# Kernel optimization log

Hardware: AMD Instinct MI355X
Metric: run time of the kernel (lower is better)

The kernel has to match this reference:

```python
import jax, jax.numpy as jnp
import numpy as np

B, N, M, C, H = 8, 1024, 128, 1024, 16
D = C // H
MLP = int(C * 4.0)
EPS = 1e-6


def setup_inputs() -> dict:
    key = jax.random.key(0)
    ks = jax.random.split(key, 24)
    def w(k, shape):
        return jax.random.normal(k, shape, jnp.float32) * 0.02
    mask = jax.random.randint(ks[3], (B, M), 0, 2, dtype=jnp.int32)
    mask = mask.at[:, 0].set(1)  # ensure at least one attendable token per row
    return {
        "x": jax.random.normal(ks[0], (B, N, C), jnp.float32),
        "c_dino": jax.random.normal(ks[1], (B, C), jnp.float32),
        "c_text": jax.random.normal(ks[2], (B, M, C), jnp.float32),
        "text_mask": mask,
        "W_ada": w(ks[4], (C, 6 * C)), "b_ada": jnp.zeros((6 * C,), jnp.float32),
        "W_qkv": w(ks[5], (C, 3 * C)), "b_qkv": jnp.zeros((3 * C,), jnp.float32),
        "W_proj_sa": w(ks[6], (C, C)), "b_proj_sa": jnp.zeros((C,), jnp.float32),
        "W_q": w(ks[7], (C, C)), "b_q": jnp.zeros((C,), jnp.float32),
        "W_kv": w(ks[8], (C, 2 * C)), "b_kv": jnp.zeros((2 * C,), jnp.float32),
        "W_proj_ca": w(ks[9], (C, C)), "b_proj_ca": jnp.zeros((C,), jnp.float32),
        "W_fc1": w(ks[10], (C, MLP)), "b_fc1": jnp.zeros((MLP,), jnp.float32),
        "W_fc2": w(ks[11], (MLP, C)), "b_fc2": jnp.zeros((C,), jnp.float32),
    }


def _ln(x):
    # LayerNorm without affine params, eps=1e-6
    mu = jnp.mean(x, axis=-1, keepdims=True)
    xc = x - mu
    var = jnp.mean(xc * xc, axis=-1, keepdims=True)
    return xc * jax.lax.rsqrt(var + EPS)


def _modulate(x, shift, scale):
    return x * (1.0 + scale[:, None, :]) + shift[:, None, :]


def _heads(t):
    b, n, _ = t.shape
    return t.reshape(b, n, H, D)


def reference(x, c_dino, c_text, text_mask,
              W_ada, b_ada, W_qkv, b_qkv, W_proj_sa, b_proj_sa,
              W_q, b_q, W_kv, b_kv, W_proj_ca, b_proj_ca,
              W_fc1, b_fc1, W_fc2, b_fc2):
    scale = D ** (-0.5)
    ada = jax.nn.silu(c_dino) @ W_ada + b_ada  # (B, 6C)
    sh_msa, sc_msa, sh_ca, sc_ca, sh_mlp, sc_mlp = jnp.split(ada, 6, axis=1)

    # --- self-attention ---
    h = _modulate(_ln(x), sh_msa, sc_msa)
    qkv = h @ W_qkv + b_qkv
    q, k, v = (_heads(t) for t in jnp.split(qkv, 3, axis=-1))  # (B,N,H,D)
    attn = jax.nn.softmax(jnp.einsum('bnhd,bmhd->bhnm', q, k) * scale, axis=-1)
    sa = jnp.einsum('bhnm,bmhd->bnhd', attn, v).reshape(B, N, C) @ W_proj_sa + b_proj_sa
    x = x + sa

    # --- cross-attention ---
    h = _modulate(_ln(x), sh_ca, sc_ca)
    q = _heads(h @ W_q + b_q)                 # (B,N,H,D)
    kv = c_text @ W_kv + b_kv
    k, v = (_heads(t) for t in jnp.split(kv, 2, axis=-1))  # (B,M,H,D)
    scores = jnp.einsum('bnhd,bmhd->bhnm', q, k) * scale
    scores = jnp.where(text_mask[:, None, None, :] == 0, -jnp.inf, scores)
    attn = jax.nn.softmax(scores, axis=-1)
    ca = jnp.einsum('bhnm,bmhd->bnhd', attn, v).reshape(B, N, C) @ W_proj_ca + b_proj_ca
    x = x + ca

    # --- MLP ---
    h = _modulate(_ln(x), sh_mlp, sc_mlp)
    mlp = jax.nn.gelu(h @ W_fc1 + b_fc1, approximate=True) @ W_fc2 + b_fc2
    return x + mlp
```

## Files before the change

kernel.cpp:

```cpp
#include <hip/hip_runtime.h>
#include <hip/hip_bf16.h>

#define B_   8
#define N_   1024
#define M_   128
#define C_   1024
#define H_   16
#define D_   64
#define MLP_ 4096

typedef __bf16 bf16;
typedef __bf16 bf16x8 __attribute__((ext_vector_type(8)));
typedef __bf16 bf16x4 __attribute__((ext_vector_type(4)));
typedef float  f32x4  __attribute__((ext_vector_type(4)));

__device__ __forceinline__ f32x4 mfma16(bf16x8 a, bf16x8 b, f32x4 c) {
    return __builtin_amdgcn_mfma_f32_16x16x32_bf16(a, b, c, 0, 0, 0);
}

__device__ __forceinline__ void gload16(const bf16* g, bf16* l) {
    __builtin_amdgcn_global_load_lds(
        (const __attribute__((address_space(1))) void*)g,
        (__attribute__((address_space(3))) void*)l, 16, 0, 0);
}

__global__ __launch_bounds__(256) void transpose_k(const float* __restrict__ W,
                                                   bf16* __restrict__ Wt,
                                                   int K, int Nc) {
    __shared__ float tile[32][33];
    const int x  = threadIdx.x & 31;
    const int y0 = threadIdx.x >> 5;
    const size_t n0 = (size_t)blockIdx.x * 32;
    const size_t k0 = (size_t)blockIdx.y * 32;
#pragma unroll
    for (int i = 0; i < 4; i++)
        tile[y0 + i * 8][x] = W[(k0 + y0 + i * 8) * Nc + n0 + x];
    __syncthreads();
#pragma unroll
    for (int i = 0; i < 4; i++)
        Wt[(n0 + y0 + i * 8) * K + k0 + x] = (bf16)tile[x][y0 + i * 8];
}

__global__ __launch_bounds__(256) void vtrans_k(const bf16* __restrict__ in, int instride,
                                                int coff, int Mk, bf16* __restrict__ outT) {
    __shared__ bf16 t[32][33];
    const int tx = threadIdx.x & 31;
    const int ty0 = threadIdx.x >> 5;
    const int m0  = blockIdx.x * 32;
    const int hd0 = blockIdx.y * 32;
    const int b   = blockIdx.z;
#pragma unroll
    for (int i = 0; i < 4; i++)
        t[ty0 + i * 8][tx] = in[((size_t)(b * Mk + m0 + ty0 + i * 8)) * instride + coff + hd0 + tx];
    __syncthreads();
#pragma unroll
    for (int i = 0; i < 4; i++)
        outT[((size_t)(b * 1024 + hd0 + ty0 + i * 8)) * Mk + m0 + tx] = t[tx][ty0 + i * 8];
}

__global__ __launch_bounds__(256) void cvt_bf16_k(const float* __restrict__ in,
                                                  bf16* __restrict__ out, int n4) {
    int i = blockIdx.x * 256 + threadIdx.x;
    if (i < n4) {
        float4 v = ((const float4*)in)[i];
        bf16x4 o;
        o[0] = (bf16)v.x; o[1] = (bf16)v.y; o[2] = (bf16)v.z; o[3] = (bf16)v.w;
        ((bf16x4*)out)[i] = o;
    }
}

__global__ __launch_bounds__(256) void ada_init_k(const float* __restrict__ bias,
                                                  float* __restrict__ ada) {
    int i = blockIdx.x * 256 + threadIdx.x;
    ada[i] = bias[i % 6144];
}

__global__ __launch_bounds__(256) void ada_k(const float* __restrict__ cdino,
                                             const float* __restrict__ W,
                                             float* __restrict__ ada) {
    __shared__ float sc[8][32];
    const int tid = threadIdx.x;
    const int k0  = blockIdx.y * 32;
    {
        float c = cdino[(tid >> 5) * 1024 + k0 + (tid & 31)];
        sc[tid >> 5][tid & 31] = c / (1.f + __expf(-c));
    }
    __syncthreads();
    const int col = blockIdx.x * 256 + tid;
    float acc[8];
#pragma unroll
    for (int b = 0; b < 8; b++) acc[b] = 0.f;
    for (int kk = 0; kk < 32; kk++) {
        float w = W[(size_t)(k0 + kk) * 6144 + col];
#pragma unroll
        for (int b = 0; b < 8; b++) acc[b] += sc[b][kk] * w;
    }
#pragma unroll
    for (int b = 0; b < 8; b++) atomicAdd(&ada[(size_t)b * 6144 + col], acc[b]);
}

__global__ __launch_bounds__(256) void ln_mod_k(const float* __restrict__ X,
                                                const float* __restrict__ ada,
                                                int shoff, int scoff,
                                                bf16* __restrict__ Hout) {
    const int row = blockIdx.x;
    const int b   = row >> 10;
    const int tid = threadIdx.x;
    const float4 v = ((const float4*)(X + (size_t)row * C_))[tid];
    float s  = v.x + v.y + v.z + v.w;
    float sq = v.x * v.x + v.y * v.y + v.z * v.z + v.w * v.w;
#pragma unroll
    for (int off = 32; off; off >>= 1) {
        s  += __shfl_xor(s,  off);
        sq += __shfl_xor(sq, off);
    }
    __shared__ float rs_[4], rq_[4];
    if ((tid & 63) == 0) { rs_[tid >> 6] = s; rq_[tid >> 6] = sq; }
    __syncthreads();
    s  = rs_[0] + rs_[1] + rs_[2] + rs_[3];
    sq = rq_[0] + rq_[1] + rq_[2] + rq_[3];
    const float mu   = s * (1.f / 1024.f);
    const float var  = sq * (1.f / 1024.f) - mu * mu;
    const float rstd = rsqrtf(var + 1e-6f);
    const float4 scv = ((const float4*)(ada + (size_t)b * 6144 + scoff))[tid];
    const float4 shv = ((const float4*)(ada + (size_t)b * 6144 + shoff))[tid];
    bf16x4 o;
    o[0] = (bf16)(((v.x - mu) * rstd) * (1.f + scv.x) + shv.x);
    o[1] = (bf16)(((v.y - mu) * rstd) * (1.f + scv.y) + shv.y);
    o[2] = (bf16)(((v.z - mu) * rstd) * (1.f + scv.z) + shv.z);
    o[3] = (bf16)(((v.w - mu) * rstd) * (1.f + scv.w) + shv.w);
    *(bf16x4*)(Hout + (size_t)row * C_ + tid * 4) = o;
}

template <int MODE>
__global__ __launch_bounds__(512, 2) void gemm256_k(const bf16* __restrict__ A,
                                                    const bf16* __restrict__ Bt,
                                                    const float* __restrict__ bias,
                                                    bf16* __restrict__ outB,
                                                    int Ncols, int K, int GX) {
    __shared__ __attribute__((aligned(16))) bf16 As[2][2][256][32];
    __shared__ __attribute__((aligned(16))) bf16 Bs[2][2][256][32];

    const int tid  = threadIdx.x;
    const int lane = tid & 63, wave = tid >> 6;
    const int lrow = lane & 15, quad = lane >> 4;
    const int wm = wave >> 2, wn = wave & 3;

    const unsigned lid = blockIdx.x;
    const unsigned cpx = gridDim.x >> 3;
    const unsigned g   = (lid & 7) * cpx + (lid >> 3);
    const size_t bm = (size_t)(g / GX) * 256;
    const size_t bn = (size_t)(g % GX) * 256;

    const int r0 = tid >> 2;
    const int cs = ((tid & 3) ^ (r0 & 3)) * 8;
    const bf16* gA0 = A  + (bm + r0) * (size_t)K + cs;
    const bf16* gA1 = gA0 + (size_t)128 * K;
    const bf16* gB0 = Bt + (bn + r0) * (size_t)K + cs;
    const bf16* gB1 = gB0 + (size_t)128 * K;

    f32x4 acc[8][4];
#pragma unroll
    for (int i = 0; i < 8; i++)
#pragma unroll
        for (int j = 0; j < 4; j++) acc[i][j] = (f32x4){0.f, 0.f, 0.f, 0.f};

    auto stage = [&](int bb, int ks, int koff) {
        bf16* la = &As[bb][ks][0][0] + wave * 512;
        bf16* lb = &Bs[bb][ks][0][0] + wave * 512;
        gload16(gA0 + koff, la);
        gload16(gA1 + koff, la + 4096);
        gload16(gB0 + koff, lb);
        gload16(gB1 + koff, lb + 4096);
    };

    const int xo = (quad ^ (lrow & 3)) * 8;

    auto compute = [&](int bb, int ks) {
        const bf16(*Ap)[32] = As[bb][ks];
        const bf16(*Bp)[32] = Bs[bb][ks];
        bf16x8 bq[4], af[8];
#pragma unroll
        for (int ni = 0; ni < 4; ni++)
            bq[ni] = *(const bf16x8*)&Bp[wn * 64 + ni * 16 + lrow][xo];
#pragma unroll
        for (int mi = 0; mi < 8; mi++)
            af[mi] = *(const bf16x8*)&Ap[wm * 128 + mi * 16 + lrow][xo];
        __builtin_amdgcn_s_barrier();
        __builtin_amdgcn_s_setprio(1);
#pragma unroll
        for (int mi = 0; mi < 8; mi++)
#pragma unroll
            for (int ni = 0; ni < 4; ni++)
                acc[mi][ni] = mfma16(af[mi], bq[ni], acc[mi][ni]);
        __builtin_amdgcn_s_setprio(0);
    };

    stage(0, 0, 0);
    stage(0, 1, 32);
    asm volatile("s_waitcnt vmcnt(4)" ::: "memory");
    __builtin_amdgcn_s_barrier();

    const int KT = K >> 6;
    for (int kt = 0; kt < KT - 1; ++kt) {
        const int b  = kt & 1;
        const int kn = (kt + 1) << 6;
        stage(b ^ 1, 0, kn);
        compute(b, 0);
        asm volatile("s_waitcnt vmcnt(4)" ::: "memory");
        __builtin_amdgcn_s_barrier();
        stage(b ^ 1, 1, kn + 32);
        compute(b, 1);
        asm volatile("s_waitcnt vmcnt(4)" ::: "memory");
        __builtin_amdgcn_s_barrier();
    }
    {
        const int b = (KT - 1) & 1;
        compute(b, 0);
        asm volatile("s_waitcnt vmcnt(0)" ::: "memory");
        __builtin_amdgcn_s_barrier();
        compute(b, 1);
    }

#pragma unroll
    for (int mi = 0; mi < 8; mi++) {
#pragma unroll
        for (int ni = 0; ni < 4; ni++) {
            const size_t gcol = bn + wn * 64 + ni * 16 + lrow;
            const float bv = bias[gcol];
#pragma unroll
            for (int r = 0; r < 4; r++) {
                const size_t grow = bm + wm * 128 + mi * 16 + quad * 4 + r;
                float v = acc[mi][ni][r] + bv;
                if (MODE == 3) {
                    float z = 1.59576912f * (v + 0.044715f * v * v * v);
                    v = v / (1.f + __expf(-z));
                }
                outB[grow * Ncols + gcol] = (bf16)v;
            }
        }
    }
}

template <int MODE, int KS>
__global__ __launch_bounds__(256 * KS) void gemm_k(const bf16* __restrict__ A,
                                                   const bf16* __restrict__ Bt,
                                                   const float* __restrict__ bias,
                                                   const float* resid,
                                                   float* outF, bf16* outB,
                                                   int Ncols, int K, int GX) {
    __shared__ __attribute__((aligned(16))) bf16 As[2][KS][128][32];
    __shared__ __attribute__((aligned(16))) bf16 Bs[2][KS][128][32];
    const int tid  = threadIdx.x & 255;
    const int grp  = threadIdx.x >> 8;
    const int lane = tid & 63, wave = tid >> 6;
    const int lrow = lane & 15, quad = lane >> 4;
    const int wm = wave >> 1, wn = wave & 1;

    const unsigned lid = blockIdx.x;
    const unsigned xcd = lid & 7, s = lid >> 3;
    const unsigned bnb = s % GX, bmb = (s / GX) * 8 + xcd;
    const size_t bm = (size_t)bmb * 128;
    const size_t bn = (size_t)bnb * 128;

    const int Kh = K / KS;
    const int prow = tid >> 2, pseg = tid & 3;
    const int gseg = pseg ^ ((prow >> 1) & 3);
    const bf16* gA0 = A  + (bm + prow) * (size_t)K + grp * Kh + gseg * 8;
    const bf16* gA1 = gA0 + (size_t)64 * K;
    const bf16* gB0 = Bt + (bn + prow) * (size_t)K + grp * Kh + gseg * 8;
    const bf16* gB1 = gB0 + (size_t)64 * K;
    const int bufoff = KS * 128 * 32;
    bf16* lA = &As[0][grp][0][0] + wave * 512;
    bf16* lB = &Bs[0][grp][0][0] + wave * 512;

    const int xoff = (quad ^ ((lrow >> 1) & 3)) * 8;

    f32x4 acc[4][4];
#pragma unroll
    for (int i = 0; i < 4; i++)
#pragma unroll
        for (int j = 0; j < 4; j++) acc[i][j] = (f32x4){0.f, 0.f, 0.f, 0.f};

    {
        gload16(gA0, lA);
        gload16(gA1, lA + 2048);
        gload16(gB0, lB);
        gload16(gB1, lB + 2048);
    }
    int p = 0;
    for (int ko = 0; ko < Kh; ko += 32) {
        __syncthreads();
        if (ko + 32 < Kh) {
            const int po = (p ^ 1) * bufoff;
            gload16(gA0 + ko + 32, lA + po);
            gload16(gA1 + ko + 32, lA + po + 2048);
            gload16(gB0 + ko + 32, lB + po);
            gload16(gB1 + ko + 32, lB + po + 2048);
        }
        const bf16(*Asp)[32] = As[p][grp];
        const bf16(*Bsp)[32] = Bs[p][grp];
        bf16x8 af[4], bfr[4];
#pragma unroll
        for (int mi = 0; mi < 4; mi++)
            af[mi] = *(const bf16x8*)&Asp[wm * 64 + mi * 16 + lrow][xoff];
#pragma unroll
        for (int ni = 0; ni < 4; ni++)
            bfr[ni] = *(const bf16x8*)&Bsp[wn * 64 + ni * 16 + lrow][xoff];
#pragma unroll
        for (int mi = 0; mi < 4; mi++)
#pragma unroll
            for (int ni = 0; ni < 4; ni++)
                acc[mi][ni] = mfma16(af[mi], bfr[ni], acc[mi][ni]);
        p ^= 1;
    }

    if constexpr (KS == 2) {
        f32x4* red = (f32x4*)&As[0][0][0][0];
#pragma unroll
        for (int rnd = 0; rnd < 4; rnd++) {
            __syncthreads();
            if (grp == 1) {
#pragma unroll
                for (int c = 0; c < 4; c++) {
                    const int idx = rnd * 4 + c;
                    red[c * 256 + tid] = acc[idx >> 2][idx & 3];
                }
            }
            __syncthreads();
            if (grp == 0) {
#pragma unroll
                for (int c = 0; c < 4; c++) {
                    const int idx = rnd * 4 + c;
                    acc[idx >> 2][idx & 3] += red[c * 256 + tid];
                }
            }
        }
    }

    if (grp == 0) {
#pragma unroll
        for (int mi = 0; mi < 4; mi++) {
#pragma unroll
            for (int ni = 0; ni < 4; ni++) {
                const size_t gcol = bn + wn * 64 + ni * 16 + lrow;
                const float bv = bias[gcol];
#pragma unroll
                for (int r = 0; r < 4; r++) {
                    const size_t grow = bm + wm * 64 + mi * 16 + quad * 4 + r;
                    const size_t idx  = grow * Ncols + gcol;
                    float v = acc[mi][ni][r] + bv;
                    if (MODE == 1) {
                        outF[idx] = v + resid[idx];
                    } else if (MODE == 2) {
                        outB[idx] = (bf16)v;
                    } else {
                        float z = 1.59576912f * (v + 0.044715f * v * v * v);
                        outB[idx] = (bf16)(v / (1.f + __expf(-z)));
                    }
                }
            }
        }
    }
}

template <bool MASKED>
__global__ __launch_bounds__(256) void attn_k(const bf16* __restrict__ Qp, int qstride,
                                              const bf16* __restrict__ Kp, int kstride,
                                              const bf16* __restrict__ Vtg,
                                              const int* __restrict__ mask, int Mk,
                                              bf16* __restrict__ O) {
    __shared__ __attribute__((aligned(16))) bf16 Kt[64][88];
    __shared__ __attribute__((aligned(16))) bf16 Vt[64][88];
    __shared__ __attribute__((aligned(16))) bf16 Pt[4][16][88];
    __shared__ float madd[64];

    const int b = blockIdx.z, h = blockIdx.y;
    const int tid  = threadIdx.x;
    const int lane = tid & 63, wave = tid >> 6;
    const int lrow = lane & 15, quad = lane >> 4;
    const int q0 = blockIdx.x * 64 + wave * 16;

    const bf16* qp = Qp + ((size_t)(b * N_ + q0 + lrow)) * qstride + h * 64 + quad * 8;
    const bf16x8 bq0 = *(const bf16x8*)(qp);
    const bf16x8 bq1 = *(const bf16x8*)(qp + 32);

    f32x4 acc[4];
#pragma unroll
    for (int t = 0; t < 4; t++) acc[t] = (f32x4){0.f, 0.f, 0.f, 0.f};
    float mrun = -3e38f, lrun = 0.f;

    const int srow = tid >> 2;
    const int sseg = (tid & 3) * 16;

    const bf16* kbase = Kp + ((size_t)b * Mk + srow) * kstride + h * 64 + sseg;
    const bf16* vbase = Vtg + ((size_t)(b * 1024 + h * 64 + srow)) * Mk + sseg;

    for (int kc = 0; kc < Mk; kc += 64) {
        __syncthreads();
        const bf16* kp = kbase + (size_t)kc * kstride;
        bf16x8 k0 = *(const bf16x8*)kp;
        bf16x8 k1 = *(const bf16x8*)(kp + 8);
        *(bf16x8*)&Kt[srow][sseg]     = k0;
        *(bf16x8*)&Kt[srow][sseg + 8] = k1;
        const bf16* vp = vbase + kc;
        bf16x8 v0 = *(const bf16x8*)vp;
        bf16x8 v1 = *(const bf16x8*)(vp + 8);
        *(bf16x8*)&Vt[srow][sseg]     = v0;
        *(bf16x8*)&Vt[srow][sseg + 8] = v1;
        if (MASKED && tid < 64)
            madd[tid] = (mask[b * Mk + kc + tid] == 0) ? -1e30f : 0.f;
        __syncthreads();

        float sv[4][4];
#pragma unroll
        for (int t = 0; t < 4; t++) {
            f32x4 s = (f32x4){0.f, 0.f, 0.f, 0.f};
            bf16x8 ak0 = *(const bf16x8*)&Kt[t * 16 + lrow][quad * 8];
            s = mfma16(ak0, bq0, s);
            bf16x8 ak1 = *(const bf16x8*)&Kt[t * 16 + lrow][32 + quad * 8];
            s = mfma16(ak1, bq1, s);
#pragma unroll
            for (int r = 0; r < 4; r++) {
                float ma = MASKED ? madd[t * 16 + quad * 4 + r] : 0.f;
                sv[t][r] = s[r] * 0.125f + ma;
            }
        }

        float vmax = sv[0][0];
#pragma unroll
        for (int t = 0; t < 4; t++)
#pragma unroll
            for (int r = 0; r < 4; r++) vmax = fmaxf(vmax, sv[t][r]);
        vmax = fmaxf(vmax, __shfl_xor(vmax, 16));
        vmax = fmaxf(vmax, __shfl_xor(vmax, 32));
        const float mnew  = fmaxf(mrun, vmax);
        const float alpha = __expf(mrun - mnew);
        mrun = mnew;
        float rsum = 0.f;
#pragma unroll
        for (int t = 0; t < 4; t++) {
            bf16x4 p4;
#pragma unroll
            for (int r = 0; r < 4; r++) {
                float p = __expf(sv[t][r] - mnew);
                rsum += p;
                p4[r] = (bf16)p;
            }
            *(bf16x4*)&Pt[wave][lrow][t * 16 + quad * 4] = p4;
        }
        rsum += __shfl_xor(rsum, 16);
        rsum += __shfl_xor(rsum, 32);
        lrun = lrun * alpha + rsum;

        float alpha4[4];
#pragma unroll
        for (int r = 0; r < 4; r++) alpha4[r] = __shfl(alpha, quad * 4 + r);
#pragma unroll
        for (int t = 0; t < 4; t++)
#pragma unroll
            for (int r = 0; r < 4; r++) acc[t][r] *= alpha4[r];

        __syncthreads();
        const bf16x8 ap0 = *(const bf16x8*)&Pt[wave][lrow][quad * 8];
        const bf16x8 ap1 = *(const bf16x8*)&Pt[wave][lrow][32 + quad * 8];

#pragma unroll
        for (int t = 0; t < 4; t++) {
            bf16x8 bv0 = *(const bf16x8*)&Vt[t * 16 + lrow][quad * 8];
            acc[t] = mfma16(ap0, bv0, acc[t]);
            bf16x8 bv1 = *(const bf16x8*)&Vt[t * 16 + lrow][32 + quad * 8];
            acc[t] = mfma16(ap1, bv1, acc[t]);
        }
    }

    float linv = 1.f / lrun;
    float linv4[4];
#pragma unroll
    for (int r = 0; r < 4; r++) linv4[r] = __shfl(linv, quad * 4 + r);
#pragma unroll
    for (int r = 0; r < 4; r++) {
        const size_t grow = (size_t)(b * N_ + q0 + quad * 4 + r);
#pragma unroll
        for (int t = 0; t < 4; t++)
            O[grow * C_ + h * 64 + t * 16 + lrow] = (bf16)(acc[t][r] * linv4[r]);
    }
}

extern "C" void kernel_launch(void* const* d_in, const int* in_sizes, int n_in,
                              void* d_out, int out_size, void* d_ws, size_t ws_size,
                              hipStream_t stream) {
    const float* x     = (const float*)d_in[0];
    const float* cdino = (const float*)d_in[1];
    const float* ctext = (const float*)d_in[2];
    const int*   tmask = (const int*)d_in[3];
    const float* W_ada = (const float*)d_in[4];
    const float* b_ada = (const float*)d_in[5];
    const float* W_qkv = (const float*)d_in[6];
    const float* b_qkv = (const float*)d_in[7];
    const float* W_sa  = (const float*)d_in[8];
    const float* b_sa  = (const float*)d_in[9];
    const float* W_q   = (const float*)d_in[10];
    const float* b_q   = (const float*)d_in[11];
    const float* W_kv  = (const float*)d_in[12];
    const float* b_kv  = (const float*)d_in[13];
    const float* W_ca  = (const float*)d_in[14];
    const float* b_ca  = (const float*)d_in[15];
    const float* W_fc1 = (const float*)d_in[16];
    const float* b_fc1 = (const float*)d_in[17];
    const float* W_fc2 = (const float*)d_in[18];
    const float* b_fc2 = (const float*)d_in[19];
    float* out = (float*)d_out;

    char* ws = (char*)d_ws;
    size_t off = 0;
    auto alloc = [&](size_t bytes) -> char* {
        char* p = ws + off;
        off += (bytes + 255) & ~(size_t)255;
        return p;
    };
    float* ada  = (float*)alloc((size_t)8 * 6144 * 4);
    bf16* ctxb  = (bf16*)alloc((size_t)1024 * 1024 * 2);
    bf16* WqkvT = (bf16*)alloc((size_t)3072 * 1024 * 2);
    bf16* WsaT  = (bf16*)alloc((size_t)1024 * 1024 * 2);
    bf16* WqT   = (bf16*)alloc((size_t)1024 * 1024 * 2);
    bf16* WkvT  = (bf16*)alloc((size_t)2048 * 1024 * 2);
    bf16* WcaT  = (bf16*)alloc((size_t)1024 * 1024 * 2);
    bf16* Wfc1T = (bf16*)alloc((size_t)4096 * 1024 * 2);
    bf16* Wfc2T = (bf16*)alloc((size_t)1024 * 4096 * 2);
    float* xbuf = (float*)alloc((size_t)8192 * 1024 * 4);
    bf16* hbuf  = (bf16*)alloc((size_t)8192 * 1024 * 2);
    bf16* attnb = (bf16*)alloc((size_t)8192 * 1024 * 2);
    bf16* VtgSA = (bf16*)alloc((size_t)8192 * 1024 * 2);
    bf16* VtgCA = (bf16*)alloc((size_t)8192 * 128 * 2);
    bf16* pool  = (bf16*)alloc((size_t)8192 * 4096 * 2);
    if (off > ws_size) return;

    bf16* qkvb  = pool;
    bf16* qb    = pool;
    bf16* kvb   = pool + (size_t)8192 * 1024;
    bf16* gelub = pool;

    transpose_k<<<dim3(3072 / 32, 1024 / 32), 256, 0, stream>>>(W_qkv, WqkvT, 1024, 3072);
    transpose_k<<<dim3(1024 / 32, 1024 / 32), 256, 0, stream>>>(W_sa,  WsaT,  1024, 1024);
    transpose_k<<<dim3(1024 / 32, 1024 / 32), 256, 0, stream>>>(W_q,   WqT,   1024, 1024);
    transpose_k<<<dim3(2048 / 32, 1024 / 32), 256, 0, stream>>>(W_kv,  WkvT,  1024, 2048);
    transpose_k<<<dim3(1024 / 32, 1024 / 32), 256, 0, stream>>>(W_ca,  WcaT,  1024, 1024);
    transpose_k<<<dim3(4096 / 32, 1024 / 32), 256, 0, stream>>>(W_fc1, Wfc1T, 1024, 4096);
    transpose_k<<<dim3(1024 / 32, 4096 / 32), 256, 0, stream>>>(W_fc2, Wfc2T, 4096, 1024);
    cvt_bf16_k<<<1024, 256, 0, stream>>>(ctext, ctxb, 262144);

    ada_init_k<<<192, 256, 0, stream>>>(b_ada, ada);
    ada_k<<<dim3(24, 32), 256, 0, stream>>>(cdino, W_ada, ada);

    ln_mod_k<<<8192, 256, 0, stream>>>(x, ada, 0, 1024, hbuf);
    gemm256_k<2><<<32 * 12, 512, 0, stream>>>(hbuf, WqkvT, b_qkv, qkvb, 3072, 1024, 12);
    vtrans_k<<<dim3(32, 32, 8), 256, 0, stream>>>(qkvb, 3072, 2048, 1024, VtgSA);
    attn_k<false><<<dim3(16, 16, 8), 256, 0, stream>>>(qkvb, 3072, qkvb + 1024, 3072, VtgSA,
                                                       nullptr, 1024, attnb);
    gemm_k<1, 2><<<8 * 64, 512, 0, stream>>>(attnb, WsaT, b_sa, x, xbuf, nullptr, 1024, 1024, 8);

    ln_mod_k<<<8192, 256, 0, stream>>>(xbuf, ada, 2048, 3072, hbuf);
    gemm_k<2, 2><<<8 * 64, 512, 0, stream>>>(hbuf, WqT, b_q, nullptr, nullptr, qb, 1024, 1024, 8);
    gemm_k<2, 2><<<16 * 8, 512, 0, stream>>>(ctxb, WkvT, b_kv, nullptr, nullptr, kvb, 2048, 1024, 16);
    vtrans_k<<<dim3(4, 32, 8), 256, 0, stream>>>(kvb, 2048, 1024, 128, VtgCA);
    attn_k<true><<<dim3(16, 16, 8), 256, 0, stream>>>(qb, 1024, kvb, 2048, VtgCA,
                                                      tmask, 128, attnb);
    gemm_k<1, 2><<<8 * 64, 512, 0, stream>>>(attnb, WcaT, b_ca, xbuf, xbuf, nullptr, 1024, 1024, 8);

    ln_mod_k<<<8192, 256, 0, stream>>>(xbuf, ada, 4096, 5120, hbuf);
    gemm256_k<3><<<32 * 16, 512, 0, stream>>>(hbuf, Wfc1T, b_fc1, gelub, 4096, 1024, 16);
    gemm_k<1, 2><<<8 * 64, 512, 0, stream>>>(gelub, Wfc2T, b_fc2, xbuf, out, nullptr, 1024, 4096, 8);
}
```

Measured before the change: 742.9 us.

## Split GEMM A-fragment reads into halves interleaved with MFMA and change LDS swizzle

The GEMM inner loop now reads B fragments and half of the A fragments, issues the MFMAs for that half, then reads the second half of A and issues the rest. Extra workgroup barriers are placed between phases to keep waves in lockstep. This lowers register pressure (4 A fragments live instead of 8) and interleaves LDS reads with matrix work. The LDS XOR swizzle is changed to use row bits 1-2 instead of 0-1, aiming to reduce bank conflicts for 16-byte reads. The extra barriers add synchronisation overhead and may limit overlap across waves.

```diff
diff --git a/kernel.cpp b/kernel.cpp
--- a/kernel.cpp
+++ b/kernel.cpp
@@ -153,7 +153,7 @@
     const size_t bn = (size_t)(g % GX) * 256;
 
     const int r0 = tid >> 2;
-    const int cs = ((tid & 3) ^ (r0 & 3)) * 8;
+    const int cs = ((tid & 3) ^ ((r0 >> 1) & 3)) * 8;
     const bf16* gA0 = A  + (bm + r0) * (size_t)K + cs;
     const bf16* gA1 = gA0 + (size_t)128 * K;
     const bf16* gB0 = Bt + (bn + r0) * (size_t)K + cs;
@@ -174,25 +174,28 @@
         gload16(gB1 + koff, lb + 4096);
     };
 
-    const int xo = (quad ^ (lrow & 3)) * 8;
-
-    auto compute = [&](int bb, int ks) {
-        const bf16(*Ap)[32] = As[bb][ks];
+    const int xo = (quad ^ ((lrow >> 1) & 3)) * 8;
+
+    bf16x8 bq[4], af[4];
+    auto readB4 = [&](int bb, int ks) {
         const bf16(*Bp)[32] = Bs[bb][ks];
-        bf16x8 bq[4], af[8];
 #pragma unroll
         for (int ni = 0; ni < 4; ni++)
             bq[ni] = *(const bf16x8*)&Bp[wn * 64 + ni * 16 + lrow][xo];
-#pragma unroll
-        for (int mi = 0; mi < 8; mi++)
-            af[mi] = *(const bf16x8*)&Ap[wm * 128 + mi * 16 + lrow][xo];
-        __builtin_amdgcn_s_barrier();
+    };
+    auto readA4 = [&](int bb, int ks, int h) {
+        const bf16(*Ap)[32] = As[bb][ks];
+#pragma unroll
+        for (int mi = 0; mi < 4; mi++)
+            af[mi] = *(const bf16x8*)&Ap[wm * 128 + h * 64 + mi * 16 + lrow][xo];
+    };
+    auto mfma16c = [&](int h) {
         __builtin_amdgcn_s_setprio(1);
 #pragma unroll
-        for (int mi = 0; mi < 8; mi++)
+        for (int mi = 0; mi < 4; mi++)
 #pragma unroll
             for (int ni = 0; ni < 4; ni++)
-                acc[mi][ni] = mfma16(af[mi], bq[ni], acc[mi][ni]);
+                acc[h * 4 + mi][ni] = mfma16(af[mi], bq[ni], acc[h * 4 + mi][ni]);
         __builtin_amdgcn_s_setprio(0);
     };
 
@@ -205,21 +208,45 @@
     for (int kt = 0; kt < KT - 1; ++kt) {
         const int b  = kt & 1;
         const int kn = (kt + 1) << 6;
+        readB4(b, 0); readA4(b, 0, 0);
         stage(b ^ 1, 0, kn);
-        compute(b, 0);
+        __builtin_amdgcn_s_barrier();
+        mfma16c(0);
+        __builtin_amdgcn_s_barrier();
+        readA4(b, 0, 1);
+        __builtin_amdgcn_s_barrier();
+        mfma16c(1);
         asm volatile("s_waitcnt vmcnt(4)" ::: "memory");
         __builtin_amdgcn_s_barrier();
+        readB4(b, 1); readA4(b, 1, 0);
         stage(b ^ 1, 1, kn + 32);
-        compute(b, 1);
+        __builtin_amdgcn_s_barrier();
+        mfma16c(0);
+        __builtin_amdgcn_s_barrier();
+        readA4(b, 1, 1);
+        __builtin_amdgcn_s_barrier();
+        mfma16c(1);
         asm volatile("s_waitcnt vmcnt(4)" ::: "memory");
         __builtin_amdgcn_s_barrier();
     }
     {
         const int b = (KT - 1) & 1;
-        compute(b, 0);
+        readB4(b, 0); readA4(b, 0, 0);
+        __builtin_amdgcn_s_barrier();
+        mfma16c(0);
+        __builtin_amdgcn_s_barrier();
+        readA4(b, 0, 1);
+        __builtin_amdgcn_s_barrier();
+        mfma16c(1);
         asm volatile("s_waitcnt vmcnt(0)" ::: "memory");
         __builtin_amdgcn_s_barrier();
-        compute(b, 1);
+        readB4(b, 1); readA4(b, 1, 0);
+        __builtin_amdgcn_s_barrier();
+        mfma16c(0);
+        __builtin_amdgcn_s_barrier();
+        readA4(b, 1, 1);
+        __builtin_amdgcn_s_barrier();
+        mfma16c(1);
     }
 
 #pragma unroll
@@ -455,7 +482,7 @@
 
         float alpha4[4];
 #pragma unroll
-        for (int r = 0; r < 4; r++) alpha4[r] = __shfl(alpha, quad * 4 + r);
+    for (int r = 0; r < 4; r++) alpha4[r] = __shfl(alpha, quad * 4 + r);
 #pragma unroll
         for (int t = 0; t < 4; t++)
 #pragma unroll
```

New measurement: 728.0 us. 2.0% less time.
